# Kernel tuning notes

Measured on AMD Instinct MI355X. Metric: run time of the kernel, lower is better.

The kernel has to match this reference:

```python
import jax, jax.numpy as jnp
import numpy as np
from jax import lax

N = 8000            # total neurons
EXC_RATIO = 0.8
P = 0.1             # internal_conn_prob
DT = 0.1            # ms
TAU_SYN = 5.0
V_TH = 20.0
V_RESET = 0.0
T_REF_STEPS = int(round(2.0 / DT))
TAU_ADAPT = 200.0
BETA_ADAPT = 1.6
J_EXC = 2.0
G_INH = 5.0
EXT_RATE_FACTOR = 3.5
TAU_M = 20.0
T_STEPS = 200


def setup_inputs() -> dict:
    rng = np.random.default_rng(42)
    n_exc = int(N * EXC_RATIO)
    c_e = max(1, int(n_exc * P))
    j_eff = J_EXC * (16.0 / c_e)
    j_inh = j_eff * G_INH
    # sparse random connectivity (pre -> post), no self loops
    mask = rng.random((N, N), dtype=np.float32) < P
    np.fill_diagonal(mask, False)
    pre, post = np.nonzero(mask)
    w = np.where(pre < n_exc, j_eff, -j_inh).astype(np.float32)
    # background Poisson drive, pre-scaled by j_eff
    nu_thr = V_TH / (j_eff * c_e * TAU_M)
    bg_rate = c_e * nu_thr * EXT_RATE_FACTOR * DT  # expected events / step
    bg = rng.poisson(bg_rate, (T_STEPS, N)).astype(np.float32) * j_eff
    tau_m = np.full((N,), TAU_M, dtype=np.float32)
    return {
        "w_vals": jnp.asarray(w),
        "bg": jnp.asarray(bg),
        "tau_m": jnp.asarray(tau_m),
        "pre_idx": jnp.asarray(pre.astype(np.int32)),
        "post_idx": jnp.asarray(post.astype(np.int32)),
    }


def reference(w_vals, bg, tau_m, pre_idx, post_idx):
    decay_v = jnp.exp(-DT / tau_m)          # [N] per-neuron membrane decay
    decay_s = jnp.float32(np.exp(-DT / TAU_SYN))
    decay_a = jnp.float32(np.exp(-DT / TAU_ADAPT))

    def step(carry, bg_t):
        v, s, a, ref, spike = carry
        # sparse synaptic matmul: I_post = sum_pre W[pre,post] * spike[pre]
        rec = jax.ops.segment_sum(w_vals * spike[pre_idx], post_idx, num_segments=N)
        s = s * decay_s + rec + bg_t
        a = a * decay_a + spike              # ALIF adaptation trace
        active = ref <= 0
        v = jnp.where(active, v * decay_v + s, V_RESET)
        thr = V_TH + BETA_ADAPT * a
        new_spike = (v >= thr) & active
        v = jnp.where(new_spike, V_RESET, v)
        ref = jnp.where(new_spike, T_REF_STEPS, jnp.maximum(ref - 1, 0))
        spike_f = new_spike.astype(v.dtype)
        return (v, s, a, ref, spike_f), (spike_f, v)

    init = (
        jnp.zeros((N,), jnp.float32),   # v
        jnp.zeros((N,), jnp.float32),   # syn trace
        jnp.zeros((N,), jnp.float32),   # adaptation
        jnp.zeros((N,), jnp.int32),     # refractory counter
        jnp.zeros((N,), jnp.float32),   # spikes at t-1
    )
    _, (spikes, vs) = lax.scan(step, init, bg)
    # [2, N]: per-neuron mean firing (spikes/step) and mean membrane potential
    return jnp.stack([spikes.mean(axis=0), vs.mean(axis=0)])
```

## Files before the change

### kernel.cpp

```cpp
#include <hip/hip_runtime.h>

#define NN      8000
#define NEXC    6400
#define TSTEPS  200
#define TREF    20
#define NBLK    64
#define TPB     1024
#define NPB     125
#define EPB     112000

typedef unsigned int u32x4 __attribute__((ext_vector_type(4)));

__device__ __forceinline__ void store_uc16(unsigned* p, u32x4 v) {
    asm volatile("global_store_dwordx4 %0, %1, off sc0 sc1"
                 :: "v"(p), "v"(v) : "memory");
}
__device__ __forceinline__ u32x4 load_uc16(unsigned* p) {
    u32x4 r;
    asm volatile("global_load_dwordx4 %0, %1, off sc0 sc1\n\t"
                 "s_waitcnt vmcnt(0)"
                 : "=v"(r) : "v"(p) : "memory");
    return r;
}

__global__ void build_rowptr(const int* __restrict__ pre, int nE, int* __restrict__ row_ptr) {
    int i = blockIdx.x * blockDim.x + threadIdx.x;
    if (i > NN) return;
    int lo = 0, hi = nE;
    while (lo < hi) {
        int mid = (lo + hi) >> 1;
        if (pre[mid] < i) lo = mid + 1; else hi = mid;
    }
    row_ptr[i] = lo;
}

__global__ void build_runs(const int* __restrict__ post, const int* __restrict__ row_ptr,
                           int* __restrict__ runs) {
    int wid  = (blockIdx.x * blockDim.x + threadIdx.x) >> 6;
    int lane = threadIdx.x & 63;
    int nw   = (gridDim.x * blockDim.x) >> 6;
    for (int p = wid; p < NN; p += nw) {
        int e0 = row_ptr[p], e1 = row_ptr[p + 1];
        int target = lane * NPB;
        int lo = e0, hi = e1;
        while (lo < hi) {
            int mid = (lo + hi) >> 1;
            if (post[mid] < target) lo = mid + 1; else hi = mid;
        }
        runs[lane * NN + p] = lo;
        if (lane == 0) runs[64 * NN + p] = e1;
    }
}

__global__ __launch_bounds__(1024) void build_brp(
    const int* __restrict__ post, const int* __restrict__ runs,
    int* __restrict__ brp, unsigned short* __restrict__ bedge)
{
    __shared__ int wsum[16];
    const int b = blockIdx.x, lt = threadIdx.x;
    const int p0 = lt * 8;
    int cnts[8]; int loc = 0;
    for (int j = 0; j < 8; ++j) {
        int p = p0 + j;
        int c = (p < NN) ? (runs[(b + 1) * NN + p] - runs[b * NN + p]) : 0;
        cnts[j] = c; loc += c;
    }
    int x = loc;
    for (int off = 1; off < 64; off <<= 1) {
        int u = __shfl_up(x, off, 64);
        if ((lt & 63) >= off) x += u;
    }
    if ((lt & 63) == 63) wsum[lt >> 6] = x;
    __syncthreads();
    if (lt < 16) {
        int y = wsum[lt];
        for (int off = 1; off < 16; off <<= 1) {
            int u = __shfl_up(y, off, 16);
            if (lt >= off) y += u;
        }
        wsum[lt] = y;
    }
    __syncthreads();
    int base = x - loc + ((lt >> 6) ? wsum[(lt >> 6) - 1] : 0);
    for (int j = 0; j < 8; ++j) {
        int p = p0 + j;
        if (p < NN) {
            brp[b * (NN + 1) + p] = base;
            int e0 = runs[b * NN + p];
            for (int k = 0; k < cnts[j]; ++k)
                bedge[(size_t)b * EPB + base + k] =
                    (unsigned short)(post[e0 + k] - b * NPB);
            base += cnts[j];
        }
    }
    if (lt == 1023) brp[b * (NN + 1) + NN] = base;
}

__global__ void init_ws(unsigned* chunks) {
    int i = blockIdx.x * blockDim.x + threadIdx.x;
    if (i < 2 * NBLK * 4) chunks[i] = 0u;
}

__global__ __launch_bounds__(TPB) void sim(
    const float* __restrict__ bg, const float* __restrict__ tau_m,
    const int* __restrict__ brp, const unsigned short* __restrict__ bedge,
    unsigned* __restrict__ chunks, float* __restrict__ out)
{
#pragma clang fp contract(off)
    __shared__ unsigned cnt[NPB];
    __shared__ unsigned mybits[4];
    __shared__ float    bg_sh[2][NPB];
    __shared__ int      list_sh[NN];
    __shared__ int      nspk_sh;

    const int b    = blockIdx.x;
    const int lt   = threadIdx.x;
    const int wave = lt >> 6;
    const int g    = b * NPB + lt;
    const bool own = (lt < NPB);
    const int* __restrict__ brp_b = brp + b * (NN + 1);
    const unsigned short* __restrict__ bedge_b = bedge + (size_t)b * EPB;

    const float JE = (float)(2.0 * (16.0 / 640.0));
    const float JI = (float)(2.0 * (16.0 / 640.0) * 5.0);
    const float DS = (float)0.98019867330675525;
    const float DA = (float)0.99950012497917929;

    float dv = 0.f, v = 0.f, s = 0.f, a = 0.f, spike = 0.f, sum_v = 0.f;
    int ref = 0, sum_spk = 0;
    if (own) {
        dv = expf(-(0.1f / tau_m[g]));
        cnt[lt] = 0u;
    }
    if (lt >= TPB - 128) {
        int j = lt - (TPB - 128);
        if (j < NPB) bg_sh[0][j] = bg[b * NPB + j];
    }
    __syncthreads();

    for (int t = 0; t < TSTEPS; ++t) {
        bool ns = false;
        if (own) {
            unsigned c = cnt[lt];
            cnt[lt] = 0u;
            float rec = (float)(c & 0xFFFFu) * JE - (float)(c >> 16) * JI;
            s = s * DS + rec + bg_sh[t & 1][lt];
            a = a * DA + spike;
            bool active = (ref <= 0);
            v = active ? (v * dv + s) : 0.f;
            float thr = 20.0f + 1.6f * a;
            ns = (v >= thr) && active;
            if (ns) v = 0.f;
            ref = ns ? TREF : (ref > 0 ? ref - 1 : 0);
            spike = ns ? 1.f : 0.f;
            sum_spk += ns ? 1 : 0;
            sum_v += v;
        }
        if (wave < 2) {
            unsigned long long bal = __ballot(ns);
            if ((lt & 63) == 0) {
                mybits[wave * 2 + 0] = (unsigned)(bal & 0xFFFFFFFFu);
                mybits[wave * 2 + 1] = (unsigned)(bal >> 32);
            }
        }
        __syncthreads();

        if (lt == 0) {
            u32x4 ch;
            ch[0] = mybits[0]; ch[1] = mybits[1]; ch[2] = mybits[2];
            ch[3] = mybits[3] | (((unsigned)((t + 1) & 7)) << 29);
            store_uc16(&chunks[((t & 1) * NBLK + b) * 4], ch);
        }
        float bgv = 0.f; int bgj = -1;
        if (lt >= TPB - 128 && (t + 1) < TSTEPS) {
            int j = lt - (TPB - 128);
            if (j < NPB) { bgj = j; bgv = bg[(t + 1) * NN + b * NPB + j]; }
        }
        if (lt < NBLK) {
            const unsigned want = ((unsigned)((t + 1) & 7)) << 29;
            u32x4 c;
            for (;;) {
                c = load_uc16(&chunks[((t & 1) * NBLK + lt) * 4]);
                if ((c[3] & 0xE0000000u) == want) break;
            }
            c[3] &= 0x1FFFFFFFu;
            int tot = __popc(c[0]) + __popc(c[1]) + __popc(c[2]) + __popc(c[3]);
            int x = tot;
            for (int off = 1; off < 64; off <<= 1) {
                int u = __shfl_up(x, off, 64);
                if (lt >= off) x += u;
            }
            int pos = x - tot;
            int base = lt * NPB;
            #pragma unroll
            for (int w = 0; w < 4; ++w) {
                unsigned wd = c[w];
                while (wd) {
                    int j = __ffs(wd) - 1;
                    wd &= wd - 1;
                    list_sh[pos++] = base + w * 32 + j;
                }
            }
            if (lt == 63) nspk_sh = x;
        }
        __syncthreads();

        const int ktot = nspk_sh;
        for (int i = lt; i < 2 * ktot; i += TPB) {
            int sp = list_sh[i >> 1];
            int o0 = brp_b[sp];
            int o1 = brp_b[sp + 1];
            int mid = (o0 + o1 + 1) >> 1;
            int s0 = (i & 1) ? mid : o0;
            int s1 = (i & 1) ? o1 : mid;
            unsigned incr = (sp < NEXC) ? 1u : 0x10000u;
            for (int e = s0; e < s1; ++e) {
                atomicAdd(&cnt[bedge_b[e]], incr);
            }
        }
        if (bgj >= 0) bg_sh[(t + 1) & 1][bgj] = bgv;
        __syncthreads();
    }

    if (own) {
        out[g]      = (float)sum_spk / 200.0f;
        out[NN + g] = sum_v / 200.0f;
    }
}

extern "C" void kernel_launch(void* const* d_in, const int* in_sizes, int n_in,
                              void* d_out, int out_size, void* d_ws, size_t ws_size,
                              hipStream_t stream) {
    const float* bg       = (const float*)d_in[1];
    const float* tau_m    = (const float*)d_in[2];
    const int*   pre_idx  = (const int*)d_in[3];
    const int*   post_idx = (const int*)d_in[4];
    const int    nE       = in_sizes[0];
    float* out = (float*)d_out;

    char* ws = (char*)d_ws;
    size_t off = 0;
    int* runs    = (int*)(ws + off);          off += (size_t)65 * NN * 4;
    int* row_ptr = (int*)(ws + off);          off += (size_t)(NN + 1) * 4;
    off = (off + 63) & ~(size_t)63;
    int* brp     = (int*)(ws + off);          off += (size_t)NBLK * (NN + 1) * 4;
    off = (off + 63) & ~(size_t)63;
    unsigned short* bedge = (unsigned short*)(ws + off); off += (size_t)NBLK * EPB * 2;
    off = (off + 63) & ~(size_t)63;
    unsigned* chunks = (unsigned*)(ws + off); off += (size_t)2 * NBLK * 16;

    hipLaunchKernelGGL(build_rowptr, dim3(32), dim3(256), 0, stream, pre_idx, nE, row_ptr);
    hipLaunchKernelGGL(build_runs, dim3(256), dim3(256), 0, stream, post_idx, row_ptr, runs);
    hipLaunchKernelGGL(build_brp, dim3(NBLK), dim3(1024), 0, stream, post_idx, runs, brp, bedge);
    hipLaunchKernelGGL(init_ws, dim3(1), dim3(512), 0, stream, chunks);
    hipLaunchKernelGGL(sim, dim3(NBLK), dim3(TPB), 0, stream,
                       bg, tau_m, brp, bedge, chunks, out);
}
```

Measured before the change: 864.9 us.

## Publish per-wave spike chunks directly to drop a per-step block barrier

Each of the two spike-owning waves now writes its own ballot mask and step tag straight to a global chunk. Before, the masks went through shared memory, then a __syncthreads, then a single-thread store. The polling wave loads both per-block chunks with one paired uncached load and checks both tags. The next-step background load is also written straight into the double-buffered shared array instead of being held in registers. Together these remove one block-wide barrier and a shared round trip from each timestep's critical path, at the cost of twice as many chunk slots to poll.

```diff
diff --git a/kernel.cpp b/kernel.cpp
--- a/kernel.cpp
+++ b/kernel.cpp
@@ -15,12 +15,12 @@
     asm volatile("global_store_dwordx4 %0, %1, off sc0 sc1"
                  :: "v"(p), "v"(v) : "memory");
 }
-__device__ __forceinline__ u32x4 load_uc16(unsigned* p) {
-    u32x4 r;
-    asm volatile("global_load_dwordx4 %0, %1, off sc0 sc1\n\t"
+__device__ __forceinline__ void load_uc16x2(unsigned* pa, unsigned* pb,
+                                            u32x4& ra, u32x4& rb) {
+    asm volatile("global_load_dwordx4 %0, %2, off sc0 sc1\n\t"
+                 "global_load_dwordx4 %1, %3, off sc0 sc1\n\t"
                  "s_waitcnt vmcnt(0)"
-                 : "=v"(r) : "v"(p) : "memory");
-    return r;
+                 : "=&v"(ra), "=&v"(rb) : "v"(pa), "v"(pb) : "memory");
 }
 
 __global__ void build_rowptr(const int* __restrict__ pre, int nE, int* __restrict__ row_ptr) {
@@ -98,7 +98,7 @@
 
 __global__ void init_ws(unsigned* chunks) {
     int i = blockIdx.x * blockDim.x + threadIdx.x;
-    if (i < 2 * NBLK * 4) chunks[i] = 0u;
+    if (i < 2 * NBLK * 2 * 4) chunks[i] = 0u;
 }
 
 __global__ __launch_bounds__(TPB) void sim(
@@ -108,7 +108,6 @@
 {
 #pragma clang fp contract(off)
     __shared__ unsigned cnt[NPB];
-    __shared__ unsigned mybits[4];
     __shared__ float    bg_sh[2][NPB];
     __shared__ int      list_sh[NN];
     __shared__ int      nspk_sh;
@@ -116,6 +115,7 @@
     const int b    = blockIdx.x;
     const int lt   = threadIdx.x;
     const int wave = lt >> 6;
+    const int lane = lt & 63;
     const int g    = b * NPB + lt;
     const bool own = (lt < NPB);
     const int* __restrict__ brp_b = brp + b * (NN + 1);
@@ -139,6 +139,8 @@
     __syncthreads();
 
     for (int t = 0; t < TSTEPS; ++t) {
+        const unsigned tag = ((unsigned)((t + 1) & 7)) << 29;
+
         bool ns = false;
         if (own) {
             unsigned c = cnt[lt];
@@ -158,50 +160,48 @@
         }
         if (wave < 2) {
             unsigned long long bal = __ballot(ns);
-            if ((lt & 63) == 0) {
-                mybits[wave * 2 + 0] = (unsigned)(bal & 0xFFFFFFFFu);
-                mybits[wave * 2 + 1] = (unsigned)(bal >> 32);
-            }
-        }
-        __syncthreads();
-
-        if (lt == 0) {
-            u32x4 ch;
-            ch[0] = mybits[0]; ch[1] = mybits[1]; ch[2] = mybits[2];
-            ch[3] = mybits[3] | (((unsigned)((t + 1) & 7)) << 29);
-            store_uc16(&chunks[((t & 1) * NBLK + b) * 4], ch);
-        }
-        float bgv = 0.f; int bgj = -1;
+            if (lane == 0) {
+                u32x4 ch;
+                ch[0] = (unsigned)(bal & 0xFFFFFFFFu);
+                ch[1] = (unsigned)(bal >> 32);
+                ch[2] = 0u;
+                ch[3] = tag;
+                store_uc16(&chunks[(((t & 1) * NBLK + b) * 2 + wave) * 4], ch);
+            }
+        }
         if (lt >= TPB - 128 && (t + 1) < TSTEPS) {
             int j = lt - (TPB - 128);
-            if (j < NPB) { bgj = j; bgv = bg[(t + 1) * NN + b * NPB + j]; }
-        }
-        if (lt < NBLK) {
-            const unsigned want = ((unsigned)((t + 1) & 7)) << 29;
-            u32x4 c;
+            if (j < NPB) bg_sh[(t + 1) & 1][j] = bg[(t + 1) * NN + b * NPB + j];
+        }
+
+        if (wave == 0) {
+            unsigned* pA = &chunks[(((t & 1) * NBLK + lane) * 2 + 0) * 4];
+            unsigned* pB = &chunks[(((t & 1) * NBLK + lane) * 2 + 1) * 4];
+            u32x4 cA, cB;
             for (;;) {
-                c = load_uc16(&chunks[((t & 1) * NBLK + lt) * 4]);
-                if ((c[3] & 0xE0000000u) == want) break;
-            }
-            c[3] &= 0x1FFFFFFFu;
-            int tot = __popc(c[0]) + __popc(c[1]) + __popc(c[2]) + __popc(c[3]);
+                load_uc16x2(pA, pB, cA, cB);
+                if (cA[3] == tag && cB[3] == tag) break;
+            }
+            unsigned w0 = cA[0], w1 = cA[1], w2 = cB[0], w3 = cB[1];
+            int tot = __popc(w0) + __popc(w1) + __popc(w2) + __popc(w3);
             int x = tot;
             for (int off = 1; off < 64; off <<= 1) {
                 int u = __shfl_up(x, off, 64);
-                if (lt >= off) x += u;
+                if (lane >= off) x += u;
             }
             int pos = x - tot;
-            int base = lt * NPB;
+            int base = lane * NPB;
+            unsigned wd[4] = {w0, w1, w2, w3};
             #pragma unroll
             for (int w = 0; w < 4; ++w) {
-                unsigned wd = c[w];
-                while (wd) {
-                    int j = __ffs(wd) - 1;
-                    wd &= wd - 1;
+                unsigned m = wd[w];
+                while (m) {
+                    int j = __ffs(m) - 1;
+                    m &= m - 1;
                     list_sh[pos++] = base + w * 32 + j;
                 }
             }
-            if (lt == 63) nspk_sh = x;
+            if (lane == 63) nspk_sh = x;
         }
         __syncthreads();
 
@@ -218,7 +218,6 @@
                 atomicAdd(&cnt[bedge_b[e]], incr);
             }
         }
-        if (bgj >= 0) bg_sh[(t + 1) & 1][bgj] = bgv;
         __syncthreads();
     }
 
@@ -247,12 +246,12 @@
     off = (off + 63) & ~(size_t)63;
     unsigned short* bedge = (unsigned short*)(ws + off); off += (size_t)NBLK * EPB * 2;
     off = (off + 63) & ~(size_t)63;
-    unsigned* chunks = (unsigned*)(ws + off); off += (size_t)2 * NBLK * 16;
+    unsigned* chunks = (unsigned*)(ws + off); off += (size_t)2 * NBLK * 2 * 16;
 
     hipLaunchKernelGGL(build_rowptr, dim3(32), dim3(256), 0, stream, pre_idx, nE, row_ptr);
     hipLaunchKernelGGL(build_runs, dim3(256), dim3(256), 0, stream, post_idx, row_ptr, runs);
     hipLaunchKernelGGL(build_brp, dim3(NBLK), dim3(1024), 0, stream, post_idx, runs, brp, bedge);
-    hipLaunchKernelGGL(init_ws, dim3(1), dim3(512), 0, stream, chunks);
+    hipLaunchKernelGGL(init_ws, dim3(1), dim3(1024), 0, stream, chunks);
     hipLaunchKernelGGL(sim, dim3(NBLK), dim3(TPB), 0, stream,
                        bg, tau_m, brp, bedge, chunks, out);
 }
```

After: 942.0 us. 8.9% more time.

## Parallelize bedge construction per edge and trim per-step spike publish path

Applied to the files above, without the earlier changes.

Moves the per-block edge-target fill out of build_brp, where each thread serially copied its runs, into a new per-edge kernel that computes each edge's destination slot from brp and runs. This spreads roughly 6.4M edge writes across many threads instead of 64 blocks. In the simulation loop, wave 1 now publishes the spike chunk using its own ballot directly, so only wave 0 writes to shared memory and the whole of wave 0 does the polling. The new fill relies on pre_idx being sorted and on each edge's position within its run matching the earlier serial order. It also adds one extra kernel launch.

```diff
diff --git a/kernel.cpp b/kernel.cpp
--- a/kernel.cpp
+++ b/kernel.cpp
@@ -53,8 +53,7 @@
 }
 
 __global__ __launch_bounds__(1024) void build_brp(
-    const int* __restrict__ post, const int* __restrict__ runs,
-    int* __restrict__ brp, unsigned short* __restrict__ bedge)
+    const int* __restrict__ runs, int* __restrict__ brp)
 {
     __shared__ int wsum[16];
     const int b = blockIdx.x, lt = threadIdx.x;
@@ -86,14 +85,23 @@
         int p = p0 + j;
         if (p < NN) {
             brp[b * (NN + 1) + p] = base;
-            int e0 = runs[b * NN + p];
-            for (int k = 0; k < cnts[j]; ++k)
-                bedge[(size_t)b * EPB + base + k] =
-                    (unsigned short)(post[e0 + k] - b * NPB);
             base += cnts[j];
         }
     }
     if (lt == 1023) brp[b * (NN + 1) + NN] = base;
+}
+
+__global__ void bedge_fill(const int* __restrict__ pre, const int* __restrict__ post,
+                           const int* __restrict__ runs, const int* __restrict__ brp,
+                           unsigned short* __restrict__ bedge, int nE)
+{
+    int e = blockIdx.x * blockDim.x + threadIdx.x;
+    if (e >= nE) return;
+    int p = pre[e];
+    int q = post[e];
+    int b = q / NPB;
+    int dst = brp[b * (NN + 1) + p] + (e - runs[b * NN + p]);
+    bedge[(size_t)b * EPB + dst] = (unsigned short)(q - b * NPB);
 }
 
 __global__ void init_ws(unsigned* chunks) {
@@ -108,7 +116,7 @@
 {
 #pragma clang fp contract(off)
     __shared__ unsigned cnt[NPB];
-    __shared__ unsigned mybits[4];
+    __shared__ unsigned mybits[2];
     __shared__ float    bg_sh[2][NPB];
     __shared__ int      list_sh[NN];
     __shared__ int      nspk_sh;
@@ -116,6 +124,7 @@
     const int b    = blockIdx.x;
     const int lt   = threadIdx.x;
     const int wave = lt >> 6;
+    const int lane = lt & 63;
     const int g    = b * NPB + lt;
     const bool own = (lt < NPB);
     const int* __restrict__ brp_b = brp + b * (NN + 1);
@@ -139,6 +148,8 @@
     __syncthreads();
 
     for (int t = 0; t < TSTEPS; ++t) {
+        const unsigned tag = ((unsigned)((t + 1) & 7)) << 29;
+
         bool ns = false;
         if (own) {
             unsigned c = cnt[lt];
@@ -156,19 +167,22 @@
             sum_spk += ns ? 1 : 0;
             sum_v += v;
         }
+        unsigned long long bal = 0ull;
         if (wave < 2) {
-            unsigned long long bal = __ballot(ns);
-            if ((lt & 63) == 0) {
-                mybits[wave * 2 + 0] = (unsigned)(bal & 0xFFFFFFFFu);
-                mybits[wave * 2 + 1] = (unsigned)(bal >> 32);
+            bal = __ballot(ns);
+            if (wave == 0 && lane == 0) {
+                mybits[0] = (unsigned)(bal & 0xFFFFFFFFu);
+                mybits[1] = (unsigned)(bal >> 32);
             }
         }
         __syncthreads();
 
-        if (lt == 0) {
+        if (lt == 64) {
             u32x4 ch;
-            ch[0] = mybits[0]; ch[1] = mybits[1]; ch[2] = mybits[2];
-            ch[3] = mybits[3] | (((unsigned)((t + 1) & 7)) << 29);
+            ch[0] = mybits[0];
+            ch[1] = mybits[1];
+            ch[2] = (unsigned)(bal & 0xFFFFFFFFu);
+            ch[3] = ((unsigned)(bal >> 32) & 0x1FFFFFFFu) | tag;
             store_uc16(&chunks[((t & 1) * NBLK + b) * 4], ch);
         }
         float bgv = 0.f; int bgj = -1;
@@ -176,32 +190,34 @@
             int j = lt - (TPB - 128);
             if (j < NPB) { bgj = j; bgv = bg[(t + 1) * NN + b * NPB + j]; }
         }
-        if (lt < NBLK) {
-            const unsigned want = ((unsigned)((t + 1) & 7)) << 29;
+
+        if (wave == 0) {
             u32x4 c;
+            unsigned* pp = &chunks[((t & 1) * NBLK + lane) * 4];
             for (;;) {
-                c = load_uc16(&chunks[((t & 1) * NBLK + lt) * 4]);
-                if ((c[3] & 0xE0000000u) == want) break;
-            }
-            c[3] &= 0x1FFFFFFFu;
-            int tot = __popc(c[0]) + __popc(c[1]) + __popc(c[2]) + __popc(c[3]);
+                c = load_uc16(pp);
+                if ((c[3] & 0xE0000000u) == tag) break;
+            }
+            unsigned w0 = c[0], w1 = c[1], w2 = c[2], w3 = c[3] & 0x1FFFFFFFu;
+            int tot = __popc(w0) + __popc(w1) + __popc(w2) + __popc(w3);
             int x = tot;
             for (int off = 1; off < 64; off <<= 1) {
                 int u = __shfl_up(x, off, 64);
-                if (lt >= off) x += u;
+                if (lane >= off) x += u;
             }
             int pos = x - tot;
-            int base = lt * NPB;
+            int base = lane * NPB;
+            unsigned wd[4] = {w0, w1, w2, w3};
             #pragma unroll
             for (int w = 0; w < 4; ++w) {
-                unsigned wd = c[w];
-                while (wd) {
-                    int j = __ffs(wd) - 1;
-                    wd &= wd - 1;
+                unsigned m = wd[w];
+                while (m) {
+                    int j = __ffs(m) - 1;
+                    m &= m - 1;
                     list_sh[pos++] = base + w * 32 + j;
                 }
             }
-            if (lt == 63) nspk_sh = x;
+            if (lane == 63) nspk_sh = x;
         }
         __syncthreads();
 
@@ -211,10 +227,10 @@
             int o0 = brp_b[sp];
             int o1 = brp_b[sp + 1];
             int mid = (o0 + o1 + 1) >> 1;
-            int s0 = (i & 1) ? mid : o0;
-            int s1 = (i & 1) ? o1 : mid;
+            int e0 = (i & 1) ? mid : o0;
+            int e1 = (i & 1) ? o1 : mid;
             unsigned incr = (sp < NEXC) ? 1u : 0x10000u;
-            for (int e = s0; e < s1; ++e) {
+            for (int e = e0; e < e1; ++e) {
                 atomicAdd(&cnt[bedge_b[e]], incr);
             }
         }
@@ -251,7 +267,9 @@
 
     hipLaunchKernelGGL(build_rowptr, dim3(32), dim3(256), 0, stream, pre_idx, nE, row_ptr);
     hipLaunchKernelGGL(build_runs, dim3(256), dim3(256), 0, stream, post_idx, row_ptr, runs);
-    hipLaunchKernelGGL(build_brp, dim3(NBLK), dim3(1024), 0, stream, post_idx, runs, brp, bedge);
+    hipLaunchKernelGGL(build_brp, dim3(NBLK), dim3(1024), 0, stream, runs, brp);
+    hipLaunchKernelGGL(bedge_fill, dim3((nE + 255) / 256), dim3(256), 0, stream,
+                       pre_idx, post_idx, runs, brp, bedge, nE);
     hipLaunchKernelGGL(init_ws, dim3(1), dim3(512), 0, stream, chunks);
     hipLaunchKernelGGL(sim, dim3(NBLK), dim3(TPB), 0, stream,
                        bg, tau_m, brp, bedge, chunks, out);
```

Measured after the change: 897.8 us. 1.04x slower.
